# Kernel tuning notes

Hardware: AMD Instinct MI355X
Metric: run time of the kernel (lower is better)

## Reference

```python
import jax, jax.numpy as jnp
from jax import lax
import numpy as np

B, T, I, H, L = 64, 512, 256, 768, 2


def setup_inputs() -> dict:
    key = jax.random.key(0)
    ks = jax.random.split(key, 1 + 4 * L)
    s = 1.0 / np.sqrt(H)
    inp = {"x": jax.random.normal(ks[0], (B, T, I), dtype=jnp.float32)}
    for l in range(L):
        in_dim = I if l == 0 else H
        k0, k1, k2, k3 = ks[1 + 4 * l: 5 + 4 * l]
        inp[f"w_ih{l}"] = jax.random.uniform(k0, (4 * H, in_dim), jnp.float32, -s, s)
        inp[f"w_hh{l}"] = jax.random.uniform(k1, (4 * H, H), jnp.float32, -s, s)
        inp[f"b_ih{l}"] = jax.random.uniform(k2, (4 * H,), jnp.float32, -s, s)
        inp[f"b_hh{l}"] = jax.random.uniform(k3, (4 * H,), jnp.float32, -s, s)
    return inp


def _lstm_layer(xs, w_ih, w_hh, b_ih, b_hh):
    # xs: [B,T,in]; precompute input projections for all timesteps at once
    gx = jnp.einsum('bti,gi->btg', xs, w_ih) + b_ih  # [B,T,4H]
    h0 = jnp.zeros((xs.shape[0], H), xs.dtype)
    c0 = jnp.zeros((xs.shape[0], H), xs.dtype)

    def step(carry, gx_t):
        h, c = carry
        g = gx_t + h @ w_hh.T + b_hh  # [B,4H]
        i_g, f_g, g_g, o_g = jnp.split(g, 4, axis=-1)  # PyTorch gate order i,f,g,o
        i_g = jax.nn.sigmoid(i_g)
        f_g = jax.nn.sigmoid(f_g)
        g_g = jnp.tanh(g_g)
        o_g = jax.nn.sigmoid(o_g)
        c = f_g * c + i_g * g_g
        h = o_g * jnp.tanh(c)
        return (h, c), h

    (h, c), ys = lax.scan(step, (h0, c0), jnp.swapaxes(gx, 0, 1))  # scan over T
    return jnp.swapaxes(ys, 0, 1), h, c  # [B,T,H], [B,H], [B,H]


def reference(x, w_ih0, w_hh0, b_ih0, b_hh0, w_ih1, w_hh1, b_ih1, b_hh1):
    params = [(w_ih0, w_hh0, b_ih0, b_hh0), (w_ih1, w_hh1, b_ih1, b_hh1)]
    hs, cs = [], []
    ys = x
    for (w_ih, w_hh, b_ih, b_hh) in params:
        ys, h, c = _lstm_layer(ys, w_ih, w_hh, b_ih, b_hh)
        hs.append(h)
        cs.append(c)
    return ys, (tuple(hs), tuple(cs))
```

## Files before the change

### kernel.cpp

```cpp
#include <hip/hip_runtime.h>
#include <math.h>


#define B_   64
#define T_   512
#define I_   256
#define H_   768
#define G4H  3072

constexpr size_t BTH = (size_t)B_ * T_ * H_;
constexpr size_t BH  = (size_t)B_ * H_;

using f16_t = _Float16;
using f16x8 = __attribute__((ext_vector_type(8))) _Float16;
using f32x4 = __attribute__((ext_vector_type(4))) float;
typedef unsigned long long u64;

#define MFMA(a, b, c) __builtin_amdgcn_mfma_f32_16x16x32_f16((a), (b), (c), 0, 0, 0)

#define SLOT_STRIDE 98304
#define RING_BYTES  (8 * SLOT_STRIDE)

#define SMEM_BYTES 132224

__global__ void k_packW(const float* __restrict__ src, f16_t* __restrict__ dst,
                        int K, int KC, int total) {
  int i = blockIdx.x * blockDim.x + threadIdx.x;
  int stride = gridDim.x * blockDim.x;
  for (; i < total; i += stride) {
    int e = i & 7;
    int lane = (i >> 3) & 63;
    int rest = i >> 9;
    int kc = rest % KC;
    int ptile = rest / KC;
    int p = ptile * 16 + (lane & 15);
    int k = kc * 32 + (lane >> 4) * 8 + e;
    int r = (p & 3) * H_ + (p >> 2);
    dst[i] = (f16_t)src[(size_t)r * K + k];
  }
}

__global__ void k_packX(const float* __restrict__ x, f16_t* __restrict__ dst) {
  int i = blockIdx.x * blockDim.x + threadIdx.x;
  int stride = gridDim.x * blockDim.x;
  const int total = 4 * T_ * 8 * 64 * 8;
  for (; i < total; i += stride) {
    int e = i & 7;
    int lane = (i >> 3) & 63;
    int kc = (i >> 9) & 7;
    int t = (i >> 12) & 511;
    int mtile = i >> 21;
    int b = mtile * 16 + (lane & 15);
    int k = kc * 32 + (lane >> 4) * 8 + e;
    dst[i] = (f16_t)x[((size_t)b * T_ + t) * I_ + k];
  }
}

__global__ void k_bias(const float* __restrict__ bih, const float* __restrict__ bhh,
                       float* __restrict__ bsum) {
  int p = blockIdx.x * blockDim.x + threadIdx.x;
  if (p < G4H) {
    int r = (p & 3) * H_ + (p >> 2);
    bsum[p] = bih[r] + bhh[r];
  }
}

__global__ void k_zero(int4* __restrict__ d, int n) {
  int i = blockIdx.x * blockDim.x + threadIdx.x;
  if (i < n) d[i] = make_int4(0, 0, 0, 0);
}

__device__ __forceinline__ float sigf(float v) {
  return __builtin_amdgcn_rcpf(1.0f + __builtin_amdgcn_exp2f(v * -1.44269504f));
}
__device__ __forceinline__ float tanhf_fast(float v) {
  return 2.0f * __builtin_amdgcn_rcpf(1.0f + __builtin_amdgcn_exp2f(v * -2.88539008f)) - 1.0f;
}

__device__ __forceinline__ u64 ld_q(const u64* p) {
  return __hip_atomic_load(p, __ATOMIC_RELAXED, __HIP_MEMORY_SCOPE_AGENT);
}
__device__ __forceinline__ unsigned ld_flag(const int* p) {
  return (unsigned)__hip_atomic_load(p, __ATOMIC_RELAXED, __HIP_MEMORY_SCOPE_AGENT);
}

template <int N>
__device__ __forceinline__ void wait_flags(const int* f, unsigned tagv) {
  const int lane = threadIdx.x & 63;
  const int* p = f + lane * 4;
  for (;;) {
    unsigned v = (lane < N) ? ld_flag(p) : tagv;
    if (__all(v == tagv)) return;
    __builtin_amdgcn_s_sleep(1);
  }
}

__device__ __forceinline__ void wait96(const int* f, unsigned tagv) {
  const int lane = threadIdx.x & 63;
  for (;;) {
    unsigned v0 = ld_flag(f + lane * 4);
    unsigned v1 = (lane < 32) ? ld_flag(f + (64 + lane) * 4) : tagv;
    if (__all((v0 == tagv) & (v1 == tagv))) return;
    __builtin_amdgcn_s_sleep(2);
  }
}

template <int KCW>
__device__ __forceinline__ void load_mfma(const char* sb, const int (&bA)[KCW],
                                          const f16_t* wl0, const f16_t* wl1,
                                          f32x4& a00, f32x4& a01, f32x4& a10,
                                          f32x4& a11) {
  u64 vA[KCW][2], vB[KCW][2];
#pragma unroll
  for (int i = 0; i < KCW; ++i) {
    const u64* p = (const u64*)(sb + bA[i]);
    vA[i][0] = ld_q(p);
    vA[i][1] = ld_q(p + 64);
    vB[i][0] = ld_q(p + 16);
    vB[i][1] = ld_q(p + 80);
  }
#pragma unroll
  for (int i = 0; i < KCW; ++i) {
    union { u64 q[2]; f16x8 f; } cA, cB;
    cA.q[0] = vA[i][0]; cA.q[1] = vA[i][1];
    cB.q[0] = vB[i][0]; cB.q[1] = vB[i][1];
    f16x8 w0 = *(const f16x8*)(wl0 + (size_t)i * 512);
    f16x8 w1 = *(const f16x8*)(wl1 + (size_t)i * 512);
    a00 = MFMA(cA.f, w0, a00);
    a01 = MFMA(cA.f, w1, a01);
    a10 = MFMA(cB.f, w0, a10);
    a11 = MFMA(cB.f, w1, a11);
  }
}

template <int KCW, bool IS_L1>
__device__ __forceinline__ void run_layer(
    int ws, const f16_t* __restrict__ Xf, const f16_t* __restrict__ Wihf,
    const f16_t* __restrict__ Whhf, const float* __restrict__ bsum,
    char* __restrict__ ring0c, char* __restrict__ ring1c,
    int* __restrict__ flag0, int* __restrict__ flag1,
    float* __restrict__ out, char* smem) {
  f16_t* WL = (f16_t*)smem;
  float (*pre)[64][33] = (float (*)[64][33])(smem + 98304);
  float* bsL = (float*)(smem + 132096);

  const int tid = threadIdx.x;
  const int wave = tid >> 6, lane = tid & 63;
  const int kg = wave & 3, mg = wave >> 2;
  const int laneo = lane * 8;
  const int pt0 = ws * 2, m0 = mg * 2;
  const int l15 = lane & 15, l4 = lane >> 4;

  if (tid < 32) bsL[tid] = bsum[ws * 32 + tid];

  if (mg == 0) {
    const f16_t* src;
    int KC, kc0;
    if constexpr (!IS_L1) {
      if (kg == 0) { src = Wihf; KC = 8;  kc0 = 0; }
      else         { src = Whhf; KC = 24; kc0 = (kg - 1) * 8; }
    } else {
      if (kg < 2)  { src = Wihf; KC = 24; kc0 = kg * 12; }
      else         { src = Whhf; KC = 24; kc0 = (kg - 2) * 12; }
    }
#pragma unroll
    for (int p = 0; p < 2; ++p)
#pragma unroll
      for (int i = 0; i < KCW; ++i)
        *(uint4*)(WL + ((size_t)((kg * 2 + p) * KCW + i)) * 512 + laneo) =
            *(const uint4*)(src + ((size_t)(pt0 + p) * KC + kc0 + i) * 512 + laneo);
  }

  int kcs = 0;
  if constexpr (!IS_L1) kcs = (kg - 1) * 8;
  else                  kcs = (kg < 2) ? kg * 12 : (kg - 2) * 12;

  int bA[KCW];
#pragma unroll
  for (int i = 0; i < KCW; ++i)
    bA[i] = ((kcs + i) * 4 + l4) * 1024 + (m0 * 16 + l15) * 8;
  const int fbase = kcs * 4;

  float c_reg = 0.f;
  const int u = tid & 7, b = tid >> 3;
  const int j = ws * 8 + u;
  char* myringc = IS_L1 ? ring1c : ring0c;
  int* myflag = IS_L1 ? flag1 : flag0;
  const f16_t* wl0 = WL + (size_t)(kg * 2) * KCW * 512 + laneo;
  const f16_t* wl1 = wl0 + (size_t)KCW * 512;

  __syncthreads();

  for (int t = 0; t < T_; ++t) {
    f32x4 a00 = {0.f, 0.f, 0.f, 0.f};
    f32x4 a01 = {0.f, 0.f, 0.f, 0.f};
    f32x4 a10 = {0.f, 0.f, 0.f, 0.f};
    f32x4 a11 = {0.f, 0.f, 0.f, 0.f};

    if constexpr (!IS_L1) {
      if (kg == 0) {
        if (mg == 1 && t >= 8)
          wait96(flag1 + (size_t)(t - 8) * 128 * 4, (unsigned)(t - 7));
        const f16_t* A0 = Xf + ((size_t)m0 * T_ + t) * 4096 + laneo;
        const f16_t* A1 = A0 + (size_t)T_ * 4096;
#pragma unroll
        for (int i = 0; i < KCW; ++i) {
          f16x8 x0 = *(const f16x8*)(A0 + (size_t)i * 512);
          f16x8 x1 = *(const f16x8*)(A1 + (size_t)i * 512);
          f16x8 w0 = *(const f16x8*)(wl0 + (size_t)i * 512);
          f16x8 w1 = *(const f16x8*)(wl1 + (size_t)i * 512);
          a00 = MFMA(x0, w0, a00);
          a01 = MFMA(x0, w1, a01);
          a10 = MFMA(x1, w0, a10);
          a11 = MFMA(x1, w1, a11);
        }
      } else if (t >= 1) {
        wait_flags<32>(flag0 + ((size_t)(t - 1) * 128 + fbase) * 4, (unsigned)t);
        const char* sb = ring0c + (size_t)((t - 1) & 7) * SLOT_STRIDE;
        load_mfma<KCW>(sb, bA, wl0, wl1, a00, a01, a10, a11);
      }
    } else {
      const int srcstep = (kg < 2) ? t : t - 1;
      if (srcstep >= 0) {
        const unsigned tg = (unsigned)(srcstep + 1);
        int* fl = (kg < 2) ? flag0 : flag1;
        wait_flags<48>(fl + ((size_t)srcstep * 128 + fbase) * 4, tg);
        const char* sb = ((kg < 2) ? ring0c : ring1c) +
                         (size_t)(srcstep & 7) * SLOT_STRIDE;
        load_mfma<KCW>(sb, bA, wl0, wl1, a00, a01, a10, a11);
      }
    }

#pragma unroll
    for (int r = 0; r < 4; ++r) {
      pre[kg][m0 * 16 + l4 * 4 + r][l15]           = a00[r];
      pre[kg][m0 * 16 + l4 * 4 + r][16 + l15]      = a01[r];
      pre[kg][m0 * 16 + 16 + l4 * 4 + r][l15]      = a10[r];
      pre[kg][m0 * 16 + 16 + l4 * 4 + r][16 + l15] = a11[r];
    }
    __syncthreads();

    float h;
    {
      float g0 = pre[0][b][4 * u + 0] + pre[1][b][4 * u + 0] + pre[2][b][4 * u + 0] + pre[3][b][4 * u + 0] + bsL[4 * u + 0];
      float g1 = pre[0][b][4 * u + 1] + pre[1][b][4 * u + 1] + pre[2][b][4 * u + 1] + pre[3][b][4 * u + 1] + bsL[4 * u + 1];
      float g2 = pre[0][b][4 * u + 2] + pre[1][b][4 * u + 2] + pre[2][b][4 * u + 2] + pre[3][b][4 * u + 2] + bsL[4 * u + 2];
      float g3 = pre[0][b][4 * u + 3] + pre[1][b][4 * u + 3] + pre[2][b][4 * u + 3] + pre[3][b][4 * u + 3] + bsL[4 * u + 3];
      float ig = sigf(g0), fg = sigf(g1), gg = tanhf_fast(g2), og = sigf(g3);
      c_reg = fg * c_reg + ig * gg;
      h = og * tanhf_fast(c_reg);

      unsigned hb = (unsigned)__builtin_bit_cast(unsigned short, (f16_t)h);
      unsigned n1 = (unsigned)__shfl((int)hb, lane + 1);
      unsigned n2 = (unsigned)__shfl((int)hb, lane + 2);
      unsigned n3 = (unsigned)__shfl((int)hb, lane + 3);
      if ((u & 3) == 0) {
        u64 val = (u64)(hb | (n1 << 16)) | ((u64)(n2 | (n3 << 16)) << 32);
        u64* dst = (u64*)(myringc + (size_t)(t & 7) * SLOT_STRIDE +
                          (size_t)ws * 1024 + (u >> 2) * 512 + (size_t)b * 8);
        __hip_atomic_store(dst, val, __ATOMIC_RELAXED, __HIP_MEMORY_SCOPE_AGENT);
      }
    }
    asm volatile("s_waitcnt vmcnt(0)" ::: "memory");
    __syncthreads();
    if (tid == 0)
      __hip_atomic_store(myflag + ((size_t)t * 128 + ws) * 4, t + 1,
                         __ATOMIC_RELAXED, __HIP_MEMORY_SCOPE_AGENT);

    if constexpr (IS_L1) {
      out[((size_t)b * T_ + t) * H_ + j] = h;
      if (t == T_ - 1) {
        out[BTH + BH + (size_t)b * H_ + j] = h;
        out[BTH + 3 * BH + (size_t)b * H_ + j] = c_reg;
      }
    } else {
      if (t == T_ - 1) {
        out[BTH + (size_t)b * H_ + j] = h;
        out[BTH + 2 * BH + (size_t)b * H_ + j] = c_reg;
      }
    }
  }
}

__launch_bounds__(512, 1)
__global__ void k_lstm(const f16_t* __restrict__ Xf,
                       const f16_t* __restrict__ Wih0f, const f16_t* __restrict__ Whh0f,
                       const f16_t* __restrict__ Wih1f, const f16_t* __restrict__ Whh1f,
                       const float* __restrict__ bsum0, const float* __restrict__ bsum1,
                       char* __restrict__ ring0c, char* __restrict__ ring1c,
                       int* __restrict__ flag0, int* __restrict__ flag1,
                       float* __restrict__ out) {
  extern __shared__ char smem[];
  const int wg = blockIdx.x;
  if (wg < 96)
    run_layer<8, false>(wg, Xf, Wih0f, Whh0f, bsum0, ring0c, ring1c, flag0, flag1, out, smem);
  else
    run_layer<12, true>(wg - 96, Xf, Wih1f, Whh1f, bsum1, ring0c, ring1c, flag0, flag1, out, smem);
}

extern "C" void kernel_launch(void* const* d_in, const int* in_sizes, int n_in,
                              void* d_out, int out_size, void* d_ws, size_t ws_size,
                              hipStream_t stream) {
  const float* x    = (const float*)d_in[0];
  const float* wih0 = (const float*)d_in[1];
  const float* whh0 = (const float*)d_in[2];
  const float* bih0 = (const float*)d_in[3];
  const float* bhh0 = (const float*)d_in[4];
  const float* wih1 = (const float*)d_in[5];
  const float* whh1 = (const float*)d_in[6];
  const float* bih1 = (const float*)d_in[7];
  const float* bhh1 = (const float*)d_in[8];
  float* out = (float*)d_out;

  char* base = (char*)d_ws;
  size_t off = 0;
  auto take = [&](size_t bytes) -> char* {
    char* r = base + off;
    off = (off + bytes + 255) & ~(size_t)255;
    return r;
  };
  f16_t* Wih0f = (f16_t*)take((size_t)G4H * I_ * 2);
  f16_t* Whh0f = (f16_t*)take((size_t)G4H * H_ * 2);
  f16_t* Wih1f = (f16_t*)take((size_t)G4H * H_ * 2);
  f16_t* Whh1f = (f16_t*)take((size_t)G4H * H_ * 2);
  f16_t* Xf    = (f16_t*)take((size_t)4 * T_ * 8 * 64 * 8 * 2);
  float* bsum0 = (float*)take((size_t)G4H * 4);
  float* bsum1 = (float*)take((size_t)G4H * 4);
  char* ring0c = take(RING_BYTES);
  char* ring1c = take(RING_BYTES);
  const size_t flagBytes = (size_t)T_ * 128 * 16;
  char* fl = take(2 * flagBytes);
  int* flag0 = (int*)fl;
  int* flag1 = flag0 + (size_t)T_ * 128 * 4;

  hipFuncSetAttribute(reinterpret_cast<const void*>(k_lstm),
                      hipFuncAttributeMaxDynamicSharedMemorySize, SMEM_BYTES);

  k_packW<<<768, 256, 0, stream>>>(wih0, Wih0f, I_, 8, G4H * I_);
  k_packW<<<2048, 256, 0, stream>>>(whh0, Whh0f, H_, 24, G4H * H_);
  k_packW<<<2048, 256, 0, stream>>>(wih1, Wih1f, H_, 24, G4H * H_);
  k_packW<<<2048, 256, 0, stream>>>(whh1, Whh1f, H_, 24, G4H * H_);
  k_packX<<<4096, 256, 0, stream>>>(x, Xf);
  k_bias<<<12, 256, 0, stream>>>(bih0, bhh0, bsum0);
  k_bias<<<12, 256, 0, stream>>>(bih1, bhh1, bsum1);
  k_zero<<<512, 256, 0, stream>>>((int4*)fl, (int)(2 * flagBytes / 16));

  k_lstm<<<192, 512, SMEM_BYTES, stream>>>(Xf, Wih0f, Whh0f, Wih1f, Whh1f,
                                           bsum0, bsum1, ring0c, ring1c,
                                           flag0, flag1, out);
}
```

Measured before the change: 2.736 ms.

## Use per-wave readiness flags with incremental consumption and deepen ring buffer

Each wave now publishes its own readiness flag right after writing its slice of h, without waiting on a workgroup barrier. Consumers poll the per-k-chunk flags and start MFMAs on each chunk as soon as it is ready, instead of waiting for all producer workgroups first. A separate per-workgroup flag, still written after the barrier, is kept for ring-slot reuse. The ring is doubled to 16 slots so the layer-0 producer can run further ahead of layer 1. The cost is more flag polling traffic, a larger flag array to zero, and a serialised load-then-compute pattern per chunk.

```diff
diff --git a/kernel.cpp b/kernel.cpp
--- a/kernel.cpp
+++ b/kernel.cpp
@@ -19,7 +19,10 @@
 #define MFMA(a, b, c) __builtin_amdgcn_mfma_f32_16x16x32_f16((a), (b), (c), 0, 0, 0)
 
 #define SLOT_STRIDE 98304
-#define RING_BYTES  (8 * SLOT_STRIDE)
+#define RING_SLOTS  16
+#define RING_BYTES  (RING_SLOTS * SLOT_STRIDE)
+
+#define WFLAG_U64S  ((size_t)T_ * 96 * 4)
 
 #define SMEM_BYTES 132224
 
@@ -84,17 +87,6 @@
   return (unsigned)__hip_atomic_load(p, __ATOMIC_RELAXED, __HIP_MEMORY_SCOPE_AGENT);
 }
 
-template <int N>
-__device__ __forceinline__ void wait_flags(const int* f, unsigned tagv) {
-  const int lane = threadIdx.x & 63;
-  const int* p = f + lane * 4;
-  for (;;) {
-    unsigned v = (lane < N) ? ld_flag(p) : tagv;
-    if (__all(v == tagv)) return;
-    __builtin_amdgcn_s_sleep(1);
-  }
-}
-
 __device__ __forceinline__ void wait96(const int* f, unsigned tagv) {
   const int lane = threadIdx.x & 63;
   for (;;) {
@@ -106,30 +98,35 @@
 }
 
 template <int KCW>
-__device__ __forceinline__ void load_mfma(const char* sb, const int (&bA)[KCW],
-                                          const f16_t* wl0, const f16_t* wl1,
-                                          f32x4& a00, f32x4& a01, f32x4& a10,
-                                          f32x4& a11) {
-  u64 vA[KCW][2], vB[KCW][2];
+__device__ __forceinline__ void consume(
+    const char* sb, const u64* wf, int kcs, int l4, int l15, int m0,
+    unsigned tagv, const f16_t* wl0, const f16_t* wl1,
+    f32x4& a00, f32x4& a01, f32x4& a10, f32x4& a11) {
+  const u64 exp = (u64)tagv * 0x100000001ULL;
 #pragma unroll
   for (int i = 0; i < KCW; ++i) {
-    const u64* p = (const u64*)(sb + bA[i]);
-    vA[i][0] = ld_q(p);
-    vA[i][1] = ld_q(p + 64);
-    vB[i][0] = ld_q(p + 16);
-    vB[i][1] = ld_q(p + 80);
-  }
-#pragma unroll
-  for (int i = 0; i < KCW; ++i) {
-    union { u64 q[2]; f16x8 f; } cA, cB;
-    cA.q[0] = vA[i][0]; cA.q[1] = vA[i][1];
-    cB.q[0] = vB[i][0]; cB.q[1] = vB[i][1];
+    const int wsP = (kcs + i) * 4 + l4;
+    const u64* f = wf + (size_t)wsP * 4 + m0;
+    for (;;) {
+      u64 f0 = ld_q(f);
+      u64 f1 = ld_q(f + 1);
+      if (__all((int)((f0 == exp) & (f1 == exp)))) break;
+    }
+    const u64* p = (const u64*)(sb + (size_t)wsP * 1024 +
+                                (size_t)(m0 * 16 + l15) * 8);
+    u64 v0 = ld_q(p);
+    u64 v1 = ld_q(p + 16);
+    u64 v2 = ld_q(p + 64);
+    u64 v3 = ld_q(p + 80);
+    union { u64 q[2]; f16x8 f8; } cA, cB;
+    cA.q[0] = v0; cA.q[1] = v2;
+    cB.q[0] = v1; cB.q[1] = v3;
     f16x8 w0 = *(const f16x8*)(wl0 + (size_t)i * 512);
     f16x8 w1 = *(const f16x8*)(wl1 + (size_t)i * 512);
-    a00 = MFMA(cA.f, w0, a00);
-    a01 = MFMA(cA.f, w1, a01);
-    a10 = MFMA(cB.f, w0, a10);
-    a11 = MFMA(cB.f, w1, a11);
+    a00 = MFMA(cA.f8, w0, a00);
+    a01 = MFMA(cA.f8, w1, a01);
+    a10 = MFMA(cB.f8, w0, a10);
+    a11 = MFMA(cB.f8, w1, a11);
   }
 }
 
@@ -138,7 +135,8 @@
     int ws, const f16_t* __restrict__ Xf, const f16_t* __restrict__ Wihf,
     const f16_t* __restrict__ Whhf, const float* __restrict__ bsum,
     char* __restrict__ ring0c, char* __restrict__ ring1c,
-    int* __restrict__ flag0, int* __restrict__ flag1,
+    u64* __restrict__ wf0, u64* __restrict__ wf1,
+    int* __restrict__ gf0, int* __restrict__ gf1,
     float* __restrict__ out, char* smem) {
   f16_t* WL = (f16_t*)smem;
   float (*pre)[64][33] = (float (*)[64][33])(smem + 98304);
@@ -175,17 +173,12 @@
   if constexpr (!IS_L1) kcs = (kg - 1) * 8;
   else                  kcs = (kg < 2) ? kg * 12 : (kg - 2) * 12;
 
-  int bA[KCW];
-#pragma unroll
-  for (int i = 0; i < KCW; ++i)
-    bA[i] = ((kcs + i) * 4 + l4) * 1024 + (m0 * 16 + l15) * 8;
-  const int fbase = kcs * 4;
-
   float c_reg = 0.f;
   const int u = tid & 7, b = tid >> 3;
   const int j = ws * 8 + u;
   char* myringc = IS_L1 ? ring1c : ring0c;
-  int* myflag = IS_L1 ? flag1 : flag0;
+  u64* mywf = IS_L1 ? wf1 : wf0;
+  int* mygf = IS_L1 ? gf1 : gf0;
   const f16_t* wl0 = WL + (size_t)(kg * 2) * KCW * 512 + laneo;
   const f16_t* wl1 = wl0 + (size_t)KCW * 512;
 
@@ -199,8 +192,9 @@
 
     if constexpr (!IS_L1) {
       if (kg == 0) {
-        if (mg == 1 && t >= 8)
-          wait96(flag1 + (size_t)(t - 8) * 128 * 4, (unsigned)(t - 7));
+        if (mg == 1 && t >= RING_SLOTS)
+          wait96(gf1 + (size_t)(t - RING_SLOTS) * 128 * 4,
+                 (unsigned)(t - RING_SLOTS + 1));
         const f16_t* A0 = Xf + ((size_t)m0 * T_ + t) * 4096 + laneo;
         const f16_t* A1 = A0 + (size_t)T_ * 4096;
 #pragma unroll
@@ -215,19 +209,18 @@
           a11 = MFMA(x1, w1, a11);
         }
       } else if (t >= 1) {
-        wait_flags<32>(flag0 + ((size_t)(t - 1) * 128 + fbase) * 4, (unsigned)t);
-        const char* sb = ring0c + (size_t)((t - 1) & 7) * SLOT_STRIDE;
-        load_mfma<KCW>(sb, bA, wl0, wl1, a00, a01, a10, a11);
+        consume<KCW>(ring0c + (size_t)((t - 1) & (RING_SLOTS - 1)) * SLOT_STRIDE,
+                     wf0 + (size_t)(t - 1) * 384, kcs, l4, l15, m0,
+                     (unsigned)t, wl0, wl1, a00, a01, a10, a11);
       }
     } else {
       const int srcstep = (kg < 2) ? t : t - 1;
       if (srcstep >= 0) {
-        const unsigned tg = (unsigned)(srcstep + 1);
-        int* fl = (kg < 2) ? flag0 : flag1;
-        wait_flags<48>(fl + ((size_t)srcstep * 128 + fbase) * 4, tg);
         const char* sb = ((kg < 2) ? ring0c : ring1c) +
-                         (size_t)(srcstep & 7) * SLOT_STRIDE;
-        load_mfma<KCW>(sb, bA, wl0, wl1, a00, a01, a10, a11);
+                         (size_t)(srcstep & (RING_SLOTS - 1)) * SLOT_STRIDE;
+        const u64* wf = ((kg < 2) ? wf0 : wf1) + (size_t)srcstep * 384;
+        consume<KCW>(sb, wf, kcs, l4, l15, m0, (unsigned)(srcstep + 1),
+                     wl0, wl1, a00, a01, a10, a11);
       }
     }
 
@@ -256,16 +249,18 @@
       unsigned n3 = (unsigned)__shfl((int)hb, lane + 3);
       if ((u & 3) == 0) {
         u64 val = (u64)(hb | (n1 << 16)) | ((u64)(n2 | (n3 << 16)) << 32);
-        u64* dst = (u64*)(myringc + (size_t)(t & 7) * SLOT_STRIDE +
+        u64* dst = (u64*)(myringc +
+                          (size_t)(t & (RING_SLOTS - 1)) * SLOT_STRIDE +
                           (size_t)ws * 1024 + (u >> 2) * 512 + (size_t)b * 8);
         __hip_atomic_store(dst, val, __ATOMIC_RELAXED, __HIP_MEMORY_SCOPE_AGENT);
       }
     }
     asm volatile("s_waitcnt vmcnt(0)" ::: "memory");
-    __syncthreads();
-    if (tid == 0)
-      __hip_atomic_store(myflag + ((size_t)t * 128 + ws) * 4, t + 1,
+    if (lane == 0) {
+      unsigned* wfp = (unsigned*)(mywf + ((size_t)t * 96 + ws) * 4 + (wave >> 1));
+      __hip_atomic_store(wfp + (wave & 1), (unsigned)(t + 1),
                          __ATOMIC_RELAXED, __HIP_MEMORY_SCOPE_AGENT);
+    }
 
     if constexpr (IS_L1) {
       out[((size_t)b * T_ + t) * H_ + j] = h;
@@ -279,6 +274,10 @@
         out[BTH + 2 * BH + (size_t)b * H_ + j] = c_reg;
       }
     }
+    __syncthreads();
+    if (tid == 0)
+      __hip_atomic_store(mygf + ((size_t)t * 128 + ws) * 4, t + 1,
+                         __ATOMIC_RELAXED, __HIP_MEMORY_SCOPE_AGENT);
   }
 }
 
@@ -288,14 +287,17 @@
                        const f16_t* __restrict__ Wih1f, const f16_t* __restrict__ Whh1f,
                        const float* __restrict__ bsum0, const float* __restrict__ bsum1,
                        char* __restrict__ ring0c, char* __restrict__ ring1c,
-                       int* __restrict__ flag0, int* __restrict__ flag1,
+                       u64* __restrict__ wf0, u64* __restrict__ wf1,
+                       int* __restrict__ gf0, int* __restrict__ gf1,
                        float* __restrict__ out) {
   extern __shared__ char smem[];
   const int wg = blockIdx.x;
   if (wg < 96)
-    run_layer<8, false>(wg, Xf, Wih0f, Whh0f, bsum0, ring0c, ring1c, flag0, flag1, out, smem);
+    run_layer<8, false>(wg, Xf, Wih0f, Whh0f, bsum0, ring0c, ring1c,
+                        wf0, wf1, gf0, gf1, out, smem);
   else
-    run_layer<12, true>(wg - 96, Xf, Wih1f, Whh1f, bsum1, ring0c, ring1c, flag0, flag1, out, smem);
+    run_layer<12, true>(wg - 96, Xf, Wih1f, Whh1f, bsum1, ring0c, ring1c,
+                        wf0, wf1, gf0, gf1, out, smem);
 }
 
 extern "C" void kernel_launch(void* const* d_in, const int* in_sizes, int n_in,
@@ -328,10 +330,14 @@
   float* bsum1 = (float*)take((size_t)G4H * 4);
   char* ring0c = take(RING_BYTES);
   char* ring1c = take(RING_BYTES);
-  const size_t flagBytes = (size_t)T_ * 128 * 16;
-  char* fl = take(2 * flagBytes);
-  int* flag0 = (int*)fl;
-  int* flag1 = flag0 + (size_t)T_ * 128 * 4;
+  const size_t wfBytes = WFLAG_U64S * 8;
+  const size_t gfBytes = (size_t)T_ * 128 * 16;
+  char* fl = take(2 * wfBytes + 2 * gfBytes);
+  u64* wf0 = (u64*)fl;
+  u64* wf1 = wf0 + WFLAG_U64S;
+  int* gf0 = (int*)(fl + 2 * wfBytes);
+  int* gf1 = gf0 + (size_t)T_ * 128 * 4;
+  const size_t zeroBytes = 2 * wfBytes + 2 * gfBytes;
 
   hipFuncSetAttribute(reinterpret_cast<const void*>(k_lstm),
                       hipFuncAttributeMaxDynamicSharedMemorySize, SMEM_BYTES);
@@ -343,9 +349,9 @@
   k_packX<<<4096, 256, 0, stream>>>(x, Xf);
   k_bias<<<12, 256, 0, stream>>>(bih0, bhh0, bsum0);
   k_bias<<<12, 256, 0, stream>>>(bih1, bhh1, bsum1);
-  k_zero<<<512, 256, 0, stream>>>((int4*)fl, (int)(2 * flagBytes / 16));
+  k_zero<<<1280, 256, 0, stream>>>((int4*)fl, (int)(zeroBytes / 16));
 
   k_lstm<<<192, 512, SMEM_BYTES, stream>>>(Xf, Wih0f, Whh0f, Wih1f, Whh1f,
                                            bsum0, bsum1, ring0c, ring1c,
-                                           flag0, flag1, out);
-}
+                                           wf0, wf1, gf0, gf1, out);
+}
```

After: 4.124 ms. 50.7% more time.

## Aggregate per-step flags into single super-flags via dedicated aggregator workgroups

Applied to the files above, without the earlier changes.

Two extra workgroups poll all 128 per-workgroup flags for each timestep and publish a single super-flag per step for each layer. Compute waves then spin on one flag instead of scanning 32–96 flags, which cuts polling traffic on the recurrent critical path. The ring buffer also grows from 8 to 16 slots to loosen the layer-1 backpressure, and the zero kernel becomes grid-stride. The cost is an extra hop of latency through the aggregator, plus the need for all 194 workgroups to be co-resident.

```diff
diff --git a/kernel.cpp b/kernel.cpp
--- a/kernel.cpp
+++ b/kernel.cpp
@@ -19,7 +19,8 @@
 #define MFMA(a, b, c) __builtin_amdgcn_mfma_f32_16x16x32_f16((a), (b), (c), 0, 0, 0)
 
 #define SLOT_STRIDE 98304
-#define RING_BYTES  (8 * SLOT_STRIDE)
+#define RING_SLOTS  16
+#define RING_BYTES  (RING_SLOTS * SLOT_STRIDE)
 
 #define SMEM_BYTES 132224
 
@@ -66,8 +67,9 @@
 }
 
 __global__ void k_zero(int4* __restrict__ d, int n) {
-  int i = blockIdx.x * blockDim.x + threadIdx.x;
-  if (i < n) d[i] = make_int4(0, 0, 0, 0);
+  int stride = gridDim.x * blockDim.x;
+  for (int i = blockIdx.x * blockDim.x + threadIdx.x; i < n; i += stride)
+    d[i] = make_int4(0, 0, 0, 0);
 }
 
 __device__ __forceinline__ float sigf(float v) {
@@ -84,24 +86,10 @@
   return (unsigned)__hip_atomic_load(p, __ATOMIC_RELAXED, __HIP_MEMORY_SCOPE_AGENT);
 }
 
-template <int N>
-__device__ __forceinline__ void wait_flags(const int* f, unsigned tagv) {
-  const int lane = threadIdx.x & 63;
-  const int* p = f + lane * 4;
+__device__ __forceinline__ void wait_super(const int* p, unsigned tagv) {
   for (;;) {
-    unsigned v = (lane < N) ? ld_flag(p) : tagv;
-    if (__all(v == tagv)) return;
+    if (ld_flag(p) == tagv) return;
     __builtin_amdgcn_s_sleep(1);
-  }
-}
-
-__device__ __forceinline__ void wait96(const int* f, unsigned tagv) {
-  const int lane = threadIdx.x & 63;
-  for (;;) {
-    unsigned v0 = ld_flag(f + lane * 4);
-    unsigned v1 = (lane < 32) ? ld_flag(f + (64 + lane) * 4) : tagv;
-    if (__all((v0 == tagv) & (v1 == tagv))) return;
-    __builtin_amdgcn_s_sleep(2);
   }
 }
 
@@ -133,12 +121,32 @@
   }
 }
 
+__device__ __forceinline__ void run_agg(const int* __restrict__ flags,
+                                        int* __restrict__ sup) {
+  if ((threadIdx.x >> 6) != 0) return;
+  const int lane = threadIdx.x & 63;
+  for (int t = 0; t < T_; ++t) {
+    const int* f = flags + (size_t)t * 128 * 4;
+    const unsigned want = (unsigned)(t + 1);
+    for (;;) {
+      unsigned v0 = ld_flag(f + lane * 4);
+      unsigned v1 = (lane < 32) ? ld_flag(f + (64 + lane) * 4) : want;
+      if (__all((v0 == want) & (v1 == want))) break;
+    }
+    asm volatile("s_waitcnt vmcnt(0)" ::: "memory");
+    if (lane == 0)
+      __hip_atomic_store(sup + (size_t)t * 4, (int)want, __ATOMIC_RELAXED,
+                         __HIP_MEMORY_SCOPE_AGENT);
+  }
+}
+
 template <int KCW, bool IS_L1>
 __device__ __forceinline__ void run_layer(
     int ws, const f16_t* __restrict__ Xf, const f16_t* __restrict__ Wihf,
     const f16_t* __restrict__ Whhf, const float* __restrict__ bsum,
     char* __restrict__ ring0c, char* __restrict__ ring1c,
     int* __restrict__ flag0, int* __restrict__ flag1,
+    int* __restrict__ sup0, int* __restrict__ sup1,
     float* __restrict__ out, char* smem) {
   f16_t* WL = (f16_t*)smem;
   float (*pre)[64][33] = (float (*)[64][33])(smem + 98304);
@@ -179,7 +187,6 @@
 #pragma unroll
   for (int i = 0; i < KCW; ++i)
     bA[i] = ((kcs + i) * 4 + l4) * 1024 + (m0 * 16 + l15) * 8;
-  const int fbase = kcs * 4;
 
   float c_reg = 0.f;
   const int u = tid & 7, b = tid >> 3;
@@ -199,8 +206,9 @@
 
     if constexpr (!IS_L1) {
       if (kg == 0) {
-        if (mg == 1 && t >= 8)
-          wait96(flag1 + (size_t)(t - 8) * 128 * 4, (unsigned)(t - 7));
+        if (mg == 1 && t >= RING_SLOTS)
+          wait_super(sup1 + (size_t)(t - RING_SLOTS) * 4,
+                     (unsigned)(t - RING_SLOTS + 1));
         const f16_t* A0 = Xf + ((size_t)m0 * T_ + t) * 4096 + laneo;
         const f16_t* A1 = A0 + (size_t)T_ * 4096;
 #pragma unroll
@@ -215,18 +223,17 @@
           a11 = MFMA(x1, w1, a11);
         }
       } else if (t >= 1) {
-        wait_flags<32>(flag0 + ((size_t)(t - 1) * 128 + fbase) * 4, (unsigned)t);
-        const char* sb = ring0c + (size_t)((t - 1) & 7) * SLOT_STRIDE;
+        wait_super(sup0 + (size_t)(t - 1) * 4, (unsigned)t);
+        const char* sb = ring0c + (size_t)((t - 1) & (RING_SLOTS - 1)) * SLOT_STRIDE;
         load_mfma<KCW>(sb, bA, wl0, wl1, a00, a01, a10, a11);
       }
     } else {
       const int srcstep = (kg < 2) ? t : t - 1;
       if (srcstep >= 0) {
         const unsigned tg = (unsigned)(srcstep + 1);
-        int* fl = (kg < 2) ? flag0 : flag1;
-        wait_flags<48>(fl + ((size_t)srcstep * 128 + fbase) * 4, tg);
+        wait_super(((kg < 2) ? sup0 : sup1) + (size_t)srcstep * 4, tg);
         const char* sb = ((kg < 2) ? ring0c : ring1c) +
-                         (size_t)(srcstep & 7) * SLOT_STRIDE;
+                         (size_t)(srcstep & (RING_SLOTS - 1)) * SLOT_STRIDE;
         load_mfma<KCW>(sb, bA, wl0, wl1, a00, a01, a10, a11);
       }
     }
@@ -256,7 +263,8 @@
       unsigned n3 = (unsigned)__shfl((int)hb, lane + 3);
       if ((u & 3) == 0) {
         u64 val = (u64)(hb | (n1 << 16)) | ((u64)(n2 | (n3 << 16)) << 32);
-        u64* dst = (u64*)(myringc + (size_t)(t & 7) * SLOT_STRIDE +
+        u64* dst = (u64*)(myringc +
+                          (size_t)(t & (RING_SLOTS - 1)) * SLOT_STRIDE +
                           (size_t)ws * 1024 + (u >> 2) * 512 + (size_t)b * 8);
         __hip_atomic_store(dst, val, __ATOMIC_RELAXED, __HIP_MEMORY_SCOPE_AGENT);
       }
@@ -289,13 +297,20 @@
                        const float* __restrict__ bsum0, const float* __restrict__ bsum1,
                        char* __restrict__ ring0c, char* __restrict__ ring1c,
                        int* __restrict__ flag0, int* __restrict__ flag1,
+                       int* __restrict__ sup0, int* __restrict__ sup1,
                        float* __restrict__ out) {
   extern __shared__ char smem[];
   const int wg = blockIdx.x;
   if (wg < 96)
-    run_layer<8, false>(wg, Xf, Wih0f, Whh0f, bsum0, ring0c, ring1c, flag0, flag1, out, smem);
+    run_layer<8, false>(wg, Xf, Wih0f, Whh0f, bsum0, ring0c, ring1c,
+                        flag0, flag1, sup0, sup1, out, smem);
+  else if (wg < 192)
+    run_layer<12, true>(wg - 96, Xf, Wih1f, Whh1f, bsum1, ring0c, ring1c,
+                        flag0, flag1, sup0, sup1, out, smem);
+  else if (wg == 192)
+    run_agg(flag0, sup0);
   else
-    run_layer<12, true>(wg - 96, Xf, Wih1f, Whh1f, bsum1, ring0c, ring1c, flag0, flag1, out, smem);
+    run_agg(flag1, sup1);
 }
 
 extern "C" void kernel_launch(void* const* d_in, const int* in_sizes, int n_in,
@@ -329,9 +344,13 @@
   char* ring0c = take(RING_BYTES);
   char* ring1c = take(RING_BYTES);
   const size_t flagBytes = (size_t)T_ * 128 * 16;
-  char* fl = take(2 * flagBytes);
+  const size_t supBytes  = (size_t)T_ * 16;
+  char* fl = take(2 * flagBytes + 2 * supBytes);
   int* flag0 = (int*)fl;
   int* flag1 = flag0 + (size_t)T_ * 128 * 4;
+  int* sup0  = flag1 + (size_t)T_ * 128 * 4;
+  int* sup1  = sup0 + (size_t)T_ * 4;
+  const size_t zeroBytes = 2 * flagBytes + 2 * supBytes;
 
   hipFuncSetAttribute(reinterpret_cast<const void*>(k_lstm),
                       hipFuncAttributeMaxDynamicSharedMemorySize, SMEM_BYTES);
@@ -343,9 +362,9 @@
   k_packX<<<4096, 256, 0, stream>>>(x, Xf);
   k_bias<<<12, 256, 0, stream>>>(bih0, bhh0, bsum0);
   k_bias<<<12, 256, 0, stream>>>(bih1, bhh1, bsum1);
-  k_zero<<<512, 256, 0, stream>>>((int4*)fl, (int)(2 * flagBytes / 16));
-
-  k_lstm<<<192, 512, SMEM_BYTES, stream>>>(Xf, Wih0f, Whh0f, Wih1f, Whh1f,
+  k_zero<<<520, 256, 0, stream>>>((int4*)fl, (int)(zeroBytes / 16));
+
+  k_lstm<<<194, 512, SMEM_BYTES, stream>>>(Xf, Wih0f, Whh0f, Wih1f, Whh1f,
                                            bsum0, bsum1, ring0c, ring1c,
-                                           flag0, flag1, out);
-}
+                                           flag0, flag1, sup0, sup1, out);
+}
```

After: 2.208 ms, median of 2. 19.3% less time.
